# Optimization experiments

Hardware: AMD Instinct MI355X
Metric: run time of the kernel (lower is better)

## Reference

```python
import jax, jax.numpy as jnp
import numpy as np

EMB_DIM = 768
NUM_HEADS = 12
OUT_DIM = 768


def setup_inputs() -> dict:
    key = jax.random.key(0)
    k_x, k_q, k_k, k_v, k_o = jax.random.split(key, 5)
    B, N, D = 8, 1024, EMB_DIM
    s = 1.0 / np.sqrt(D)
    return {
        "x": jax.random.normal(k_x, (B, N, D), dtype=jnp.float32),
        # torch nn.Linear weights are stored [out_features, in_features]
        "Wq": jax.random.normal(k_q, (D, D), dtype=jnp.float32) * s,
        "Wk": jax.random.normal(k_k, (D, D), dtype=jnp.float32) * s,
        "Wv": jax.random.normal(k_v, (D, D), dtype=jnp.float32) * s,
        "Wo": jax.random.normal(k_o, (OUT_DIM, D), dtype=jnp.float32) * s,
    }


def _split_heads(t, H):
    # [B, N, D] -> [B*H, N, D//H]  (heads folded into batch, per einsum 'b i d')
    B, N, D = t.shape
    return t.reshape(B, N, H, D // H).transpose(0, 2, 1, 3).reshape(B * H, N, D // H)


def _merge_heads(t, B, H):
    BH, N, dh = t.shape
    return t.reshape(B, H, N, dh).transpose(0, 2, 1, 3).reshape(B, N, H * dh)


def reference(x, Wq, Wk, Wv, Wo):
    B, N, D = x.shape
    H = NUM_HEADS
    dh = D // H
    # q/k/v projections (torch Linear: y = x @ W.T, no bias)
    q = _split_heads(x @ Wq.T, H)
    k = _split_heads(x @ Wk.T, H)
    v = _split_heads(x @ Wv.T, H)
    scale = dh ** (-0.5)
    # dots: 'b i d , b j d -> b i j' -> full [B*H, N, N] score matrix
    dots = jnp.einsum('bid,bjd->bij', q, k) * scale
    attn = jax.nn.softmax(dots, axis=-1)
    # dropout p=0.0 -> identity
    # vect: 'b i d , b d j -> b i j' == attn @ v
    vect = jnp.einsum('bij,bjd->bid', attn, v)
    out = _merge_heads(vect, B, H) @ Wo.T
    return out
```

## Files before the change

kernel.cpp:

```cpp
#include <hip/hip_runtime.h>
#include <hip/hip_bf16.h>
#include <stdint.h>


typedef __bf16 bf16x8 __attribute__((ext_vector_type(8)));
typedef __bf16 bf16x4 __attribute__((ext_vector_type(4)));
typedef float f32x4 __attribute__((ext_vector_type(4)));

#define GAS __attribute__((address_space(1)))
#define LAS __attribute__((address_space(3)))

__device__ __forceinline__ void glds16(const short* gp, short* lp) {
  __builtin_amdgcn_global_load_lds((const GAS void*)gp, (LAS void*)lp, 16, 0, 0);
}

__device__ __forceinline__ float fast_exp2(float x) {
#if __has_builtin(__builtin_amdgcn_exp2f)
  return __builtin_amdgcn_exp2f(x);
#else
  return __expf(x * 0.6931471805599453f);
#endif
}

__device__ __forceinline__ short bfbits(float f) {
  __bf16 b = (__bf16)f;
  union { __bf16 b; short s; } cv; cv.b = b;
  return cv.s;
}

__device__ __forceinline__ void stage8_f32(const float* __restrict__ src, short* dst) {
  float4 f0 = ((const float4*)src)[0];
  float4 f1 = ((const float4*)src)[1];
  bf16x8 t;
  t[0] = (__bf16)f0.x; t[1] = (__bf16)f0.y; t[2] = (__bf16)f0.z; t[3] = (__bf16)f0.w;
  t[4] = (__bf16)f1.x; t[5] = (__bf16)f1.y; t[6] = (__bf16)f1.z; t[7] = (__bf16)f1.w;
  *(bf16x8*)dst = t;
}

__global__ __launch_bounds__(256) void convert_kernel(
    const float* __restrict__ x, const float* __restrict__ Wq,
    const float* __restrict__ Wk, const float* __restrict__ Wv,
    const float* __restrict__ Wo,
    short* __restrict__ xb, short* __restrict__ wqkv, short* __restrict__ wob) {
  int u0 = blockIdx.x * 1024 + threadIdx.x;
#pragma unroll
  for (int i = 0; i < 4; ++i) {
    int u = u0 + i * 256;
    const float* src; short* dst;
    if (u < 786432) { src = x + (size_t)u * 8; dst = xb + (size_t)u * 8; }
    else if (u < 1007616) {
      int r = u - 786432;
      int wsel = r / 73728, off = r % 73728;
      const float* W = (wsel == 0) ? Wq : (wsel == 1) ? Wk : Wv;
      src = W + (size_t)off * 8;
      dst = wqkv + (size_t)r * 8;
    } else {
      int r = u - 1007616;
      src = Wo + (size_t)r * 8; dst = wob + (size_t)r * 8;
    }
    stage8_f32(src, dst);
  }
}

__device__ __forceinline__ void stage_half(const short* __restrict__ g, short* l,
                                           int w, int lane) {
#pragma unroll
  for (int p = 0; p < 2; ++p) {
    int c = (w * 2 + p) * 64 + lane;
    int row = c >> 3;
    int cs = ((c & 7) ^ (row & 7)) * 8;
    glds16(g + (size_t)row * 768 + cs, l + c * 8);
  }
}

__device__ __forceinline__ void stage_b192(const short* __restrict__ g, short* l,
                                           int w, int lane) {
#pragma unroll
  for (int p = 0; p < 3; ++p) {
    int c = (w * 3 + p) * 64 + lane;
    int row = c >> 3;
    int cs = ((c & 7) ^ (row & 7)) * 8;
    glds16(g + (size_t)row * 768 + cs, l + c * 8);
  }
}

__device__ __forceinline__ void bar_fence() {
  asm volatile("" ::: "memory");
  __builtin_amdgcn_s_barrier();
  asm volatile("" ::: "memory");
}

__device__ __forceinline__ void load_a8(const short* base, int wr, int l16, int quad,
                                        bf16x8 (&fa)[4][2]) {
#pragma unroll
  for (int mf = 0; mf < 4; ++mf)
#pragma unroll
    for (int kk = 0; kk < 2; ++kk) {
      int row = wr * 64 + mf * 16 + l16;
      fa[mf][kk] = *(const bf16x8*)&base[row * 64 + ((((kk << 2) + quad) ^ (row & 7)) << 3)];
    }
}

__device__ __forceinline__ void load_b4(const short* base, int rbase, int l16, int quad,
                                        bf16x8 (&fb)[2][2]) {
#pragma unroll
  for (int nf = 0; nf < 2; ++nf)
#pragma unroll
    for (int kk = 0; kk < 2; ++kk) {
      int row = rbase + nf * 16 + l16;
      fb[nf][kk] = *(const bf16x8*)&base[row * 64 + ((((kk << 2) + quad) ^ (row & 7)) << 3)];
    }
}

__device__ __forceinline__ void load_b2(const short* base, int rbase, int l16, int quad,
                                        bf16x8 (&fb)[2]) {
#pragma unroll
  for (int kk = 0; kk < 2; ++kk) {
    int row = rbase + l16;
    fb[kk] = *(const bf16x8*)&base[row * 64 + ((((kk << 2) + quad) ^ (row & 7)) << 3)];
  }
}

__device__ __forceinline__ void mma16(const bf16x8 (&fa)[4][2], const bf16x8 (&fb)[2][2],
                                      f32x4 (&acc)[4][4], int nf0) {
  __builtin_amdgcn_s_setprio(1);
#pragma unroll
  for (int kk = 0; kk < 2; ++kk)
#pragma unroll
    for (int mf = 0; mf < 4; ++mf)
#pragma unroll
      for (int nf = 0; nf < 2; ++nf)
        acc[mf][nf0 + nf] = __builtin_amdgcn_mfma_f32_16x16x32_bf16(
            fa[mf][kk], fb[nf][kk], acc[mf][nf0 + nf], 0, 0, 0);
  __builtin_amdgcn_s_setprio(0);
}

__device__ __forceinline__ void mma16o(const bf16x8 (&fa)[4][2], const bf16x8 (&fb)[2][2],
                                       f32x4 (&acc)[4][3]) {
  __builtin_amdgcn_s_setprio(1);
#pragma unroll
  for (int kk = 0; kk < 2; ++kk)
#pragma unroll
    for (int mf = 0; mf < 4; ++mf)
#pragma unroll
      for (int nf = 0; nf < 2; ++nf)
        acc[mf][nf] = __builtin_amdgcn_mfma_f32_16x16x32_bf16(
            fa[mf][kk], fb[nf][kk], acc[mf][nf], 0, 0, 0);
  __builtin_amdgcn_s_setprio(0);
}

__device__ __forceinline__ void mma8o(const bf16x8 (&fa)[4][2], const bf16x8 (&fb)[2],
                                      f32x4 (&acc)[4][3]) {
  __builtin_amdgcn_s_setprio(1);
#pragma unroll
  for (int kk = 0; kk < 2; ++kk)
#pragma unroll
    for (int mf = 0; mf < 4; ++mf)
      acc[mf][2] = __builtin_amdgcn_mfma_f32_16x16x32_bf16(
          fa[mf][kk], fb[kk], acc[mf][2], 0, 0, 0);
  __builtin_amdgcn_s_setprio(0);
}

__global__ __launch_bounds__(512, 2) void gemm_qkv(
    const short* __restrict__ xb, const short* __restrict__ wqkv,
    short* __restrict__ q, short* __restrict__ k, short* __restrict__ vt) {
  const int lin = blockIdx.x;
  const int xcd = lin & 7, grp = lin >> 3;
  const int by = grp >> 3;
  const int bx = xcd * 8 + (grp & 7);
  const int m0 = bx * 128;
  const int n0g = by * 256;
  const int tid = threadIdx.x;
  const int w = tid >> 6, lane = tid & 63, l16 = lane & 15, quad = lane >> 4;
  const int wr = w >> 2, wc = w & 3;

  __shared__ short lds[3][24576];

  const short* Asrc = xb + (size_t)m0 * 768;
  const short* Bsrc = wqkv + (size_t)n0g * 768;

  f32x4 acc[4][4];
#pragma unroll
  for (int i = 0; i < 4; ++i)
#pragma unroll
    for (int j = 0; j < 4; ++j) acc[i][j] = (f32x4){0.f, 0.f, 0.f, 0.f};

  stage_half(Asrc, &lds[0][0], w, lane);
  stage_half(Bsrc, &lds[0][8192], w, lane);
  stage_half(Bsrc + 98304, &lds[0][16384], w, lane);
  stage_half(Asrc + 64, &lds[1][0], w, lane);
  stage_half(Bsrc + 64, &lds[1][8192], w, lane);
  stage_half(Bsrc + 98304 + 64, &lds[1][16384], w, lane);
  asm volatile("s_waitcnt vmcnt(6)" ::: "memory");
  bar_fence();

  const int bh = wc >> 1;
  const int rb0 = (wc & 1) * 64;

  bf16x8 fa[4][2], fb0[2][2], fb1[2][2];

#pragma unroll
  for (int t = 0; t < 12; ++t) {
    const int buf = t % 3, nb = (t + 2) % 3;
    const bool pf = (t < 10);
    const short* A = &lds[buf][0];
    const short* Bb = &lds[buf][8192 + bh * 8192];

    load_a8(A, wr, l16, quad, fa);
    load_b4(Bb, rb0, l16, quad, fb0);
    if (pf) {
      stage_half(Asrc + (size_t)(t + 2) * 64, &lds[nb][0], w, lane);
      stage_half(Bsrc + (size_t)(t + 2) * 64, &lds[nb][8192], w, lane);
    }
    bar_fence();
    __builtin_amdgcn_sched_barrier(0);
    mma16(fa, fb0, acc, 0);
    __builtin_amdgcn_sched_barrier(0);
    bar_fence();

    load_b4(Bb, rb0 + 32, l16, quad, fb1);
    if (pf) {
      stage_half(Bsrc + 98304 + (size_t)(t + 2) * 64, &lds[nb][16384], w, lane);
      asm volatile("s_waitcnt vmcnt(6)" ::: "memory");
    } else if (t == 10) {
      asm volatile("s_waitcnt vmcnt(0)" ::: "memory");
    }
    bar_fence();
    __builtin_amdgcn_sched_barrier(0);
    mma16(fa, fb1, acc, 2);
    __builtin_amdgcn_sched_barrier(0);
    bar_fence();
  }

  const int wsel = by / 3;
  const int nl0 = (by % 3) * 256 + wc * 64;
  if (wsel == 2) {
#pragma unroll
    for (int mf = 0; mf < 4; ++mf)
#pragma unroll
      for (int nf = 0; nf < 4; ++nf) {
        int token = m0 + wr * 64 + mf * 16 + quad * 4;
        int nl = nl0 + nf * 16 + l16;
        int bhh = (token >> 10) * 12 + (nl >> 6);
        short tmp[4];
#pragma unroll
        for (int r = 0; r < 4; ++r) tmp[r] = bfbits(acc[mf][nf][r]);
        *(uint2*)(vt + (size_t)bhh * 65536 + (size_t)(nl & 63) * 1024 + (token & 1023)) =
            *(const uint2*)tmp;
      }
  } else {
    short* C = wsel ? k : q;
    const float sc = wsel ? 1.0f : 0.1803368801111244f;
#pragma unroll
    for (int mf = 0; mf < 4; ++mf)
#pragma unroll
      for (int nf = 0; nf < 4; ++nf)
#pragma unroll
        for (int r = 0; r < 4; ++r) {
          int row = m0 + wr * 64 + mf * 16 + quad * 4 + r;
          int nl = nl0 + nf * 16 + l16;
          C[(size_t)row * 768 + nl] = bfbits(acc[mf][nf][r] * sc);
        }
  }
}

__device__ __forceinline__ void attn_stage_k(const short* __restrict__ kb, int j0,
                                             short* sK, int w, int lane) {
#pragma unroll
  for (int p = 0; p < 4; ++p) {
    int lin = (w * 4 + p) * 64 + lane;
    int row = lin >> 3;
    int cs = ((lin & 7) ^ (row & 7)) * 8;
    glds16(kb + (size_t)(j0 + row) * 768 + cs, &sK[lin * 8]);
  }
}

__device__ __forceinline__ void attn_stage_v(const short* __restrict__ vb, int j0,
                                             short* sVt, int w, int lane) {
#pragma unroll
  for (int p = 0; p < 4; ++p) {
    int lin = (w * 4 + p) * 64 + lane;
    int row = lin >> 4;
    int c = lin & 15;
    int cs = (c ^ (row & 15)) * 8;
    glds16(vb + (size_t)row * 1024 + j0 + cs, &sVt[lin * 8]);
  }
}

__global__ __launch_bounds__(256, 3) void attn_kernel(
    const short* __restrict__ q, const short* __restrict__ k,
    const short* __restrict__ vt, short* __restrict__ vect) {
  const int bh = blockIdx.x % 96;
  const int qt = blockIdx.x / 96;
  const int b = bh / 12, h = bh % 12;
  const int m0 = qt * 128;
  const int tid = threadIdx.x;
  const int w = tid >> 6, lane = tid & 63, l16 = lane & 15, quad = lane >> 4;

  __shared__ short sK[128 * 64];
  __shared__ short sVt[64 * 128];

  const size_t base = (size_t)b * 786432 + (size_t)h * 64;
  const short* kb = k + base;
  const short* vb = vt + (size_t)bh * 65536;

#pragma unroll
  for (int p = 0; p < 4; ++p) {
    int lin = (w * 4 + p) * 64 + lane;
    int row = lin >> 3;
    int cs = ((lin & 7) ^ (row & 7)) * 8;
    glds16(q + base + (size_t)(m0 + row) * 768 + cs, &sK[lin * 8]);
  }
  asm volatile("s_waitcnt vmcnt(0)" ::: "memory");
  bar_fence();
  bf16x8 bq[2][2];
#pragma unroll
  for (int g = 0; g < 2; ++g)
#pragma unroll
    for (int kk = 0; kk < 2; ++kk) {
      int row = g * 64 + w * 16 + l16;
      bq[g][kk] = *(const bf16x8*)&sK[row * 64 + (((kk * 4 + quad) ^ (row & 7)) << 3)];
    }
  asm volatile("s_waitcnt lgkmcnt(0)" ::: "memory");
  __builtin_amdgcn_sched_barrier(0);
  bar_fence();

  attn_stage_k(kb, 0, sK, w, lane);
  attn_stage_v(vb, 0, sVt, w, lane);

  f32x4 l4[2];
  l4[0] = (f32x4){0.f, 0.f, 0.f, 0.f};
  l4[1] = (f32x4){0.f, 0.f, 0.f, 0.f};
  f32x4 oacc[2][4];
#pragma unroll
  for (int g = 0; g < 2; ++g)
#pragma unroll
    for (int td = 0; td < 4; ++td) oacc[g][td] = (f32x4){0.f, 0.f, 0.f, 0.f};

  for (int jt = 0; jt < 8; ++jt) {
    const int j0 = jt * 128;
    asm volatile("s_waitcnt vmcnt(4)" ::: "memory");
    bar_fence();

    bf16x4 pb[2][2][4];
#pragma unroll
    for (int jh = 0; jh < 2; ++jh) {
      f32x4 s[2][4];
#pragma unroll
      for (int g = 0; g < 2; ++g)
#pragma unroll
        for (int ti = 0; ti < 4; ++ti) s[g][ti] = (f32x4){0.f, 0.f, 0.f, 0.f};
      __builtin_amdgcn_s_setprio(1);
#pragma unroll
      for (int kk = 0; kk < 2; ++kk)
#pragma unroll
        for (int ti = 0; ti < 4; ++ti) {
          int row = jh * 64 + ti * 16 + l16;
          bf16x8 a = *(const bf16x8*)&sK[row * 64 + (((kk * 4 + quad) ^ (row & 7)) << 3)];
          s[0][ti] = __builtin_amdgcn_mfma_f32_16x16x32_bf16(a, bq[0][kk], s[0][ti], 0, 0, 0);
          s[1][ti] = __builtin_amdgcn_mfma_f32_16x16x32_bf16(a, bq[1][kk], s[1][ti], 0, 0, 0);
        }
      __builtin_amdgcn_s_setprio(0);
#pragma unroll
      for (int g = 0; g < 2; ++g)
#pragma unroll
        for (int ti = 0; ti < 4; ++ti) {
          f32x4 e;
          e[0] = fast_exp2(s[g][ti][0]);
          e[1] = fast_exp2(s[g][ti][1]);
          e[2] = fast_exp2(s[g][ti][2]);
          e[3] = fast_exp2(s[g][ti][3]);
          l4[g] += e;
          bf16x4 tb;
          tb[0] = (__bf16)e[0]; tb[1] = (__bf16)e[1];
          tb[2] = (__bf16)e[2]; tb[3] = (__bf16)e[3];
          pb[jh][g][ti] = tb;
        }
    }
    asm volatile("s_waitcnt lgkmcnt(0)" ::: "memory");
    __builtin_amdgcn_sched_barrier(0);
    bar_fence();
    if (jt < 7) attn_stage_k(kb, j0 + 128, sK, w, lane);

    if (jt < 7) { asm volatile("s_waitcnt vmcnt(4)" ::: "memory"); }
    else        { asm volatile("s_waitcnt vmcnt(0)" ::: "memory"); }
    bar_fence();

    __builtin_amdgcn_s_setprio(1);
#pragma unroll
    for (int jh = 0; jh < 2; ++jh)
#pragma unroll
      for (int t2 = 0; t2 < 2; ++t2) {
        union { bf16x4 hh[2]; bf16x8 v; } bp0, bp1;
        bp0.hh[0] = pb[jh][0][2 * t2];
        bp0.hh[1] = pb[jh][0][2 * t2 + 1];
        bp1.hh[0] = pb[jh][1][2 * t2];
        bp1.hh[1] = pb[jh][1][2 * t2 + 1];
#pragma unroll
        for (int td = 0; td < 4; ++td) {
          int row = td * 16 + l16;
          int o1 = jh * 64 + t2 * 32 + quad * 4;
          int c1 = o1 >> 3, w1 = o1 & 7;
          int c2 = c1 + 2;
          union { uint2 u[2]; bf16x8 v; } tmp;
          tmp.u[0] = *(const uint2*)&sVt[row * 128 + ((c1 ^ (row & 15)) << 3) + w1];
          tmp.u[1] = *(const uint2*)&sVt[row * 128 + ((c2 ^ (row & 15)) << 3) + w1];
          oacc[0][td] = __builtin_amdgcn_mfma_f32_16x16x32_bf16(tmp.v, bp0.v, oacc[0][td], 0, 0, 0);
          oacc[1][td] = __builtin_amdgcn_mfma_f32_16x16x32_bf16(tmp.v, bp1.v, oacc[1][td], 0, 0, 0);
        }
      }
    __builtin_amdgcn_s_setprio(0);
    asm volatile("s_waitcnt lgkmcnt(0)" ::: "memory");
    __builtin_amdgcn_sched_barrier(0);
    bar_fence();
    if (jt < 7) attn_stage_v(vb, j0 + 128, sVt, w, lane);
  }

#pragma unroll
  for (int g = 0; g < 2; ++g) {
    float l = (l4[g][0] + l4[g][1]) + (l4[g][2] + l4[g][3]);
    l += __shfl_xor(l, 16);
    l += __shfl_xor(l, 32);
    float inv = 1.0f / l;
    int i_tok = m0 + g * 64 + w * 16 + l16;
#pragma unroll
    for (int td = 0; td < 4; ++td) {
      short tmp[4];
#pragma unroll
      for (int r = 0; r < 4; ++r) tmp[r] = bfbits(oacc[g][td][r] * inv);
      *(uint2*)(vect + base + (size_t)i_tok * 768 + td * 16 + quad * 4) = *(const uint2*)tmp;
    }
  }
}

__global__ __launch_bounds__(512, 2) void gemm_out(
    const short* __restrict__ vect, const short* __restrict__ wob,
    float* __restrict__ out) {
  const int lin = blockIdx.x;
  const int xcd = lin & 7, grp = lin >> 3;
  const int by = grp >> 3;
  const int bx = xcd * 8 + (grp & 7);
  const int m0 = bx * 128;
  const int n0g = by * 192;
  const int tid = threadIdx.x;
  const int w = tid >> 6, lane = tid & 63, l16 = lane & 15, quad = lane >> 4;
  const int wr = w >> 2, wc = w & 3;

  __shared__ short lds[3][20480];

  const short* Asrc = vect + (size_t)m0 * 768;
  const short* Bsrc = wob + (size_t)n0g * 768;

  f32x4 acc[4][3];
#pragma unroll
  for (int i = 0; i < 4; ++i)
#pragma unroll
    for (int j = 0; j < 3; ++j) acc[i][j] = (f32x4){0.f, 0.f, 0.f, 0.f};

  stage_half(Asrc, &lds[0][0], w, lane);
  stage_b192(Bsrc, &lds[0][8192], w, lane);
  stage_half(Asrc + 64, &lds[1][0], w, lane);
  stage_b192(Bsrc + 64, &lds[1][8192], w, lane);
  asm volatile("s_waitcnt vmcnt(5)" ::: "memory");
  bar_fence();

  const int rb0 = wc * 48;
  bf16x8 fa[4][2], fb01[2][2], fb2[2];

#pragma unroll
  for (int t = 0; t < 12; ++t) {
    const int buf = t % 3, nb = (t + 2) % 3;
    const bool pf = (t < 10);
    const short* A = &lds[buf][0];
    const short* Bb = &lds[buf][8192];

    load_a8(A, wr, l16, quad, fa);
    load_b4(Bb, rb0, l16, quad, fb01);
    if (pf) stage_half(Asrc + (size_t)(t + 2) * 64, &lds[nb][0], w, lane);
    bar_fence();
    __builtin_amdgcn_sched_barrier(0);
    mma16o(fa, fb01, acc);
    __builtin_amdgcn_sched_barrier(0);
    bar_fence();

    load_b2(Bb, rb0 + 32, l16, quad, fb2);
    if (pf) {
      stage_b192(Bsrc + (size_t)(t + 2) * 64, &lds[nb][8192], w, lane);
      asm volatile("s_waitcnt vmcnt(5)" ::: "memory");
    } else if (t == 10) {
      asm volatile("s_waitcnt vmcnt(0)" ::: "memory");
    }
    bar_fence();
    __builtin_amdgcn_sched_barrier(0);
    mma8o(fa, fb2, acc);
    __builtin_amdgcn_sched_barrier(0);
    bar_fence();
  }

#pragma unroll
  for (int mf = 0; mf < 4; ++mf)
#pragma unroll
    for (int nf = 0; nf < 3; ++nf)
#pragma unroll
      for (int r = 0; r < 4; ++r) {
        int row = m0 + wr * 64 + mf * 16 + quad * 4 + r;
        int col = n0g + wc * 48 + nf * 16 + l16;
        out[(size_t)row * 768 + col] = acc[mf][nf][r];
      }
}

extern "C" void kernel_launch(void* const* d_in, const int* in_sizes, int n_in,
                              void* d_out, int out_size, void* d_ws, size_t ws_size,
                              hipStream_t stream) {
  const float* x  = (const float*)d_in[0];
  const float* Wq = (const float*)d_in[1];
  const float* Wk = (const float*)d_in[2];
  const float* Wv = (const float*)d_in[3];
  const float* Wo = (const float*)d_in[4];
  float* out = (float*)d_out;

  const size_t MN = (size_t)8192 * 768;
  short* q    = (short*)d_ws;
  short* k    = q + MN;
  short* vt   = k + MN;
  short* vect = q;
  short* wob  = vt + MN;

  short* xb   = (short*)d_out;
  short* wqkv = xb + MN;

  convert_kernel<<<1056, 256, 0, stream>>>(x, Wq, Wk, Wv, Wo, xb, wqkv, wob);
  gemm_qkv<<<576, 512, 0, stream>>>(xb, wqkv, q, k, vt);
  attn_kernel<<<768, 256, 0, stream>>>(q, k, vt, vect);
  gemm_out<<<256, 512, 0, stream>>>(vect, wob, out);
}
```

Measured before the change: 176.1 us.

## Pre-tile V into MFMA fragment order and simplify QKV GEMM to single-buffered

The QKV GEMM epilogue now writes V directly in a per-128-token tile layout matching the attention kernel's MFMA A-fragment order. The attention kernel can then stage V with contiguous copies and read each fragment with a single 16-byte LDS load instead of two swizzled 8-byte loads. Separately, the GEMM drops its triple-buffered prefetch pipeline for a single-buffered loop with __syncthreads and raises the occupancy hint to 4 blocks. Less LDS per block may allow more concurrent blocks, but global loads no longer overlap with MFMA work inside a block.

```diff
diff --git a/kernel.cpp b/kernel.cpp
--- a/kernel.cpp
+++ b/kernel.cpp
@@ -161,7 +161,7 @@
   __builtin_amdgcn_s_setprio(0);
 }
 
-__global__ __launch_bounds__(512, 2) void gemm_qkv(
+__global__ __launch_bounds__(512, 4) void gemm_qkv(
     const short* __restrict__ xb, const short* __restrict__ wqkv,
     short* __restrict__ q, short* __restrict__ k, short* __restrict__ vt) {
   const int lin = blockIdx.x;
@@ -174,7 +174,8 @@
   const int w = tid >> 6, lane = tid & 63, l16 = lane & 15, quad = lane >> 4;
   const int wr = w >> 2, wc = w & 3;
 
-  __shared__ short lds[3][24576];
+  __shared__ short sA[8192];
+  __shared__ short sB[16384];
 
   const short* Asrc = xb + (size_t)m0 * 768;
   const short* Bsrc = wqkv + (size_t)n0g * 768;
@@ -185,51 +186,21 @@
 #pragma unroll
     for (int j = 0; j < 4; ++j) acc[i][j] = (f32x4){0.f, 0.f, 0.f, 0.f};
 
-  stage_half(Asrc, &lds[0][0], w, lane);
-  stage_half(Bsrc, &lds[0][8192], w, lane);
-  stage_half(Bsrc + 98304, &lds[0][16384], w, lane);
-  stage_half(Asrc + 64, &lds[1][0], w, lane);
-  stage_half(Bsrc + 64, &lds[1][8192], w, lane);
-  stage_half(Bsrc + 98304 + 64, &lds[1][16384], w, lane);
-  asm volatile("s_waitcnt vmcnt(6)" ::: "memory");
-  bar_fence();
-
   const int bh = wc >> 1;
   const int rb0 = (wc & 1) * 64;
 
-  bf16x8 fa[4][2], fb0[2][2], fb1[2][2];
-
-#pragma unroll
   for (int t = 0; t < 12; ++t) {
-    const int buf = t % 3, nb = (t + 2) % 3;
-    const bool pf = (t < 10);
-    const short* A = &lds[buf][0];
-    const short* Bb = &lds[buf][8192 + bh * 8192];
-
-    load_a8(A, wr, l16, quad, fa);
-    load_b4(Bb, rb0, l16, quad, fb0);
-    if (pf) {
-      stage_half(Asrc + (size_t)(t + 2) * 64, &lds[nb][0], w, lane);
-      stage_half(Bsrc + (size_t)(t + 2) * 64, &lds[nb][8192], w, lane);
-    }
-    bar_fence();
-    __builtin_amdgcn_sched_barrier(0);
+    __syncthreads();
+    stage_half(Asrc + (size_t)t * 64, sA, w, lane);
+    stage_half(Bsrc + (size_t)t * 64, sB, w, lane);
+    stage_half(Bsrc + 98304 + (size_t)t * 64, &sB[8192], w, lane);
+    __syncthreads();
+    bf16x8 fa[4][2], fb0[2][2], fb1[2][2];
+    load_a8(sA, wr, l16, quad, fa);
+    load_b4(&sB[bh * 8192], rb0, l16, quad, fb0);
     mma16(fa, fb0, acc, 0);
-    __builtin_amdgcn_sched_barrier(0);
-    bar_fence();
-
-    load_b4(Bb, rb0 + 32, l16, quad, fb1);
-    if (pf) {
-      stage_half(Bsrc + 98304 + (size_t)(t + 2) * 64, &lds[nb][16384], w, lane);
-      asm volatile("s_waitcnt vmcnt(6)" ::: "memory");
-    } else if (t == 10) {
-      asm volatile("s_waitcnt vmcnt(0)" ::: "memory");
-    }
-    bar_fence();
-    __builtin_amdgcn_sched_barrier(0);
+    load_b4(&sB[bh * 8192], rb0 + 32, l16, quad, fb1);
     mma16(fa, fb1, acc, 2);
-    __builtin_amdgcn_sched_barrier(0);
-    bar_fence();
   }
 
   const int wsel = by / 3;
@@ -242,11 +213,13 @@
         int token = m0 + wr * 64 + mf * 16 + quad * 4;
         int nl = nl0 + nf * 16 + l16;
         int bhh = (token >> 10) * 12 + (nl >> 6);
+        int jt = (token >> 7) & 7;
+        int fb = (wr * 2 + (mf >> 1)) * 4 + nf;
         short tmp[4];
 #pragma unroll
         for (int r = 0; r < 4; ++r) tmp[r] = bfbits(acc[mf][nf][r]);
-        *(uint2*)(vt + (size_t)bhh * 65536 + (size_t)(nl & 63) * 1024 + (token & 1023)) =
-            *(const uint2*)tmp;
+        *(uint2*)(vt + (size_t)bhh * 65536 + jt * 8192 + fb * 512 +
+                  (l16 + 16 * quad) * 8 + (mf & 1) * 4) = *(const uint2*)tmp;
       }
   } else {
     short* C = wsel ? k : q;
@@ -275,15 +248,12 @@
   }
 }
 
-__device__ __forceinline__ void attn_stage_v(const short* __restrict__ vb, int j0,
+__device__ __forceinline__ void attn_stage_v(const short* __restrict__ vb, int jt,
                                              short* sVt, int w, int lane) {
 #pragma unroll
   for (int p = 0; p < 4; ++p) {
-    int lin = (w * 4 + p) * 64 + lane;
-    int row = lin >> 4;
-    int c = lin & 15;
-    int cs = (c ^ (row & 15)) * 8;
-    glds16(vb + (size_t)row * 1024 + j0 + cs, &sVt[lin * 8]);
+    int c = (w * 4 + p) * 64 + lane;
+    glds16(vb + (size_t)jt * 8192 + (size_t)c * 8, &sVt[c * 8]);
   }
 }
 
@@ -338,7 +308,6 @@
     for (int td = 0; td < 4; ++td) oacc[g][td] = (f32x4){0.f, 0.f, 0.f, 0.f};
 
   for (int jt = 0; jt < 8; ++jt) {
-    const int j0 = jt * 128;
     asm volatile("s_waitcnt vmcnt(4)" ::: "memory");
     bar_fence();
 
@@ -380,7 +349,7 @@
     asm volatile("s_waitcnt lgkmcnt(0)" ::: "memory");
     __builtin_amdgcn_sched_barrier(0);
     bar_fence();
-    if (jt < 7) attn_stage_k(kb, j0 + 128, sK, w, lane);
+    if (jt < 7) attn_stage_k(kb, (jt + 1) * 128, sK, w, lane);
 
     if (jt < 7) { asm volatile("s_waitcnt vmcnt(4)" ::: "memory"); }
     else        { asm volatile("s_waitcnt vmcnt(0)" ::: "memory"); }
@@ -396,24 +365,19 @@
         bp0.hh[1] = pb[jh][0][2 * t2 + 1];
         bp1.hh[0] = pb[jh][1][2 * t2];
         bp1.hh[1] = pb[jh][1][2 * t2 + 1];
+        const int fb = (jh * 2 + t2) * 4;
 #pragma unroll
         for (int td = 0; td < 4; ++td) {
-          int row = td * 16 + l16;
-          int o1 = jh * 64 + t2 * 32 + quad * 4;
-          int c1 = o1 >> 3, w1 = o1 & 7;
-          int c2 = c1 + 2;
-          union { uint2 u[2]; bf16x8 v; } tmp;
-          tmp.u[0] = *(const uint2*)&sVt[row * 128 + ((c1 ^ (row & 15)) << 3) + w1];
-          tmp.u[1] = *(const uint2*)&sVt[row * 128 + ((c2 ^ (row & 15)) << 3) + w1];
-          oacc[0][td] = __builtin_amdgcn_mfma_f32_16x16x32_bf16(tmp.v, bp0.v, oacc[0][td], 0, 0, 0);
-          oacc[1][td] = __builtin_amdgcn_mfma_f32_16x16x32_bf16(tmp.v, bp1.v, oacc[1][td], 0, 0, 0);
+          bf16x8 av = *(const bf16x8*)&sVt[(fb + td) * 512 + lane * 8];
+          oacc[0][td] = __builtin_amdgcn_mfma_f32_16x16x32_bf16(av, bp0.v, oacc[0][td], 0, 0, 0);
+          oacc[1][td] = __builtin_amdgcn_mfma_f32_16x16x32_bf16(av, bp1.v, oacc[1][td], 0, 0, 0);
         }
       }
     __builtin_amdgcn_s_setprio(0);
     asm volatile("s_waitcnt lgkmcnt(0)" ::: "memory");
     __builtin_amdgcn_sched_barrier(0);
     bar_fence();
-    if (jt < 7) attn_stage_v(vb, j0 + 128, sVt, w, lane);
+    if (jt < 7) attn_stage_v(vb, jt + 1, sVt, w, lane);
   }
 
 #pragma unroll
```

Result: faster. 170.5 us (-3.2%).
